# Kernel tuning notes

Hardware: AMD Instinct MI355X
Metric: run time of the kernel (lower is better)

Reference implementation:

```python
import jax, jax.numpy as jnp
import numpy as np

T = 0.2


def _cdist(a, b):
    # Euclidean cdist with zero-safe sqrt (grad 0 at coincident points, like torch)
    d2 = (a * a).sum(-1)[:, None] + (b * b).sum(-1)[None, :] - 2.0 * (a @ b.T)
    d2 = jnp.maximum(d2, 0.0)
    safe = jnp.where(d2 > 0, d2, 1.0)
    return jnp.where(d2 > 0, jnp.sqrt(safe), 0.0)


def _generator(eps, W_in, b_in, W_blk, b_blk, W_out, b_out):
    x = eps @ W_in.T + b_in
    for i in range(W_blk.shape[0]):  # 4 residual MLP blocks
        x = x + jax.nn.relu(x @ W_blk[i].T + b_blk[i])
    return x @ W_out.T + b_out


def setup_inputs() -> dict:
    N, D, H = 4096, 128, 512
    key = jax.random.key(0)
    ks = jax.random.split(key, 16)

    def lin(kw, kb, fan_in, shape_w, shape_b):
        bound = 1.0 / np.sqrt(fan_in)
        W = jax.random.uniform(kw, shape_w, jnp.float32, -bound, bound)
        b = jax.random.uniform(kb, shape_b, jnp.float32, -bound, bound)
        return W, b

    W_in, b_in = lin(ks[0], ks[1], D, (H, D), (H,))
    W_blk, b_blk = lin(ks[2], ks[3], H, (4, H, H), (4, H))
    W_out, b_out = lin(ks[4], ks[5], H, (D, H), (D,))
    y_pos = jax.random.normal(ks[6], (N, D), jnp.float32)
    eps = jax.random.normal(ks[7], (N, D), jnp.float32)
    return {"y_pos": y_pos, "eps": eps, "W_in": W_in, "b_in": b_in,
            "W_blk": W_blk, "b_blk": b_blk, "W_out": W_out, "b_out": b_out}


def reference(y_pos, eps, W_in, b_in, W_blk, b_blk, W_out, b_out):
    x = _generator(eps, W_in, b_in, W_blk, b_blk, W_out, b_out)  # [N, D]
    N = y_pos.shape[0]
    dist_pos = _cdist(x, y_pos)                                   # [N, N]
    dist_neg = _cdist(x, x) + jnp.eye(x.shape[0], dtype=x.dtype) * 1e6
    A = jnp.concatenate([-dist_pos / T, -dist_neg / T], axis=-1)  # [N, 2N]
    A_row = jax.nn.softmax(A, axis=-1)
    A_col = jax.nn.softmax(A, axis=-2)
    A_soft = jnp.sqrt(A_row * A_col)
    A_pos = A_soft[:, :N]
    A_neg = A_soft[:, N:]
    s_pos = A_pos.sum(axis=1, keepdims=True)
    s_neg = A_neg.sum(axis=1, keepdims=True)
    Wpos = A_pos * s_neg
    # torch in-place: Wpos *= s_neg mutates A_pos BEFORE A_pos.sum is taken,
    # so Wneg = A_neg * (A_pos * s_neg).sum(1) = A_neg * s_pos * s_neg
    Wneg = A_neg * (s_pos * s_neg)
    V = Wpos @ y_pos - Wneg @ x                                   # drifting field
    target = jax.lax.stop_gradient(x + V)
    return jnp.mean((x - target) ** 2)
```

## Files before the change

### kernel.cpp

```cpp
#include <hip/hip_runtime.h>
#include <math.h>

#define N 4096
#define D 128
#define H 512
#define KSPLIT 4
#define SC_LOG2 7.2134752044f

typedef short bf16x8 __attribute__((ext_vector_type(8)));
typedef float f32x4 __attribute__((ext_vector_type(4)));
typedef unsigned short u16x8 __attribute__((ext_vector_type(8)));
typedef unsigned short u16;
typedef _Float16 f16;
typedef _Float16 f16x4 __attribute__((ext_vector_type(4)));

#define MFMA(a, b, c) __builtin_amdgcn_mfma_f32_16x16x32_bf16((a), (b), (c), 0, 0, 0)

__device__ __forceinline__ float fexp2(float x)
{
#if __has_builtin(__builtin_amdgcn_exp2f)
    return __builtin_amdgcn_exp2f(x);
#else
    return exp2f(x);
#endif
}

__device__ __forceinline__ float fsqrt(float x)
{
#if __has_builtin(__builtin_amdgcn_sqrtf)
    return __builtin_amdgcn_sqrtf(x);
#else
    return sqrtf(x);
#endif
}

__device__ __forceinline__ float bf2f(u16 h)
{
    return __uint_as_float(((unsigned)h) << 16);
}

__device__ __forceinline__ u16 rtn_bf16(float v)
{
    unsigned u = __float_as_uint(v);
    return (u16)((u + 0x7FFFu + ((u >> 16) & 1u)) >> 16);
}

__device__ __forceinline__ void split1(float v, u16& h, u16& l)
{
    u16 hh = rtn_bf16(v);
    float r = v - bf2f(hh);
    h = hh;
    l = rtn_bf16(r);
}

__device__ __forceinline__ void split1_trunc(float v, u16& h, u16& l)
{
    unsigned bv = __float_as_uint(v);
    unsigned hb = bv & 0xFFFF0000u;
    float r = v - __uint_as_float(hb);
    h = (u16)(hb >> 16);
    l = (u16)(__float_as_uint(r) >> 16);
}

template <int CTRL>
__device__ __forceinline__ float dppf(float x)
{
    int r = __builtin_amdgcn_update_dpp(0, __float_as_int(x), CTRL, 0xF, 0xF, true);
    return __int_as_float(r);
}

struct SplitDesc { const float* src; u16* h; int n; int ks; int os; };
struct SplitArgs { SplitDesc d[4]; };

__global__ __launch_bounds__(256) void split_multi(SplitArgs args)
{
    SplitDesc de = args.d[blockIdx.y];
    int idx = (blockIdx.x * 256 + threadIdx.x) * 4;
    if (idx >= de.n) return;
    float4 v = *(const float4*)(de.src + idx);
    ushort4 hv;
    hv.x = rtn_bf16(v.x); hv.y = rtn_bf16(v.y);
    hv.z = rtn_bf16(v.z); hv.w = rtn_bf16(v.w);
    if (de.ks < 0) {
        *(ushort4*)(de.h + idx) = hv;
    } else {
        const int ks = de.ks, os = de.os;
        const int lsz = 1 << (ks + os);
        const int layer = idx >> (ks + os);
        const int fl = idx & (lsz - 1);
        const int col = fl >> ks;
        const int k = fl & ((1 << ks) - 1);
        const int kt = k >> 5, quad = (k >> 3) & 3, j = k & 7;
        const int pidx = layer * lsz + (((((kt << 2) + quad) << os) + col) << 3) + j;
        *(ushort4*)(de.h + pidx) = hv;
    }
}

template <int K, bool RR>
__device__ __forceinline__ void gen_layer(
    u16 (&XhS)[16][520], u16 (&XlS)[16][520],
    const u16* __restrict__ Wp, const float* __restrict__ bias,
    int w, int quad, int l16)
{
    const int nb = w * 32;
    constexpr int NT = K >> 5;
    f32x4 acc[2] = {};
    float bl2[2];
    bl2[0] = bias[nb + l16];
    bl2[1] = bias[nb + 16 + l16];
    const u16* wb = Wp + (size_t)quad * 4096 + (size_t)nb * 8 + (size_t)l16 * 8;
    #pragma unroll
    for (int kc = 0; kc < NT / 2; ++kc) {
        const int kta = 2 * kc, ktb = 2 * kc + 1;
        bf16x8 b0[2], b1[2];
        b0[0] = *(const bf16x8*)(wb + kta * 16384);
        b0[1] = *(const bf16x8*)(wb + kta * 16384 + 128);
        b1[0] = *(const bf16x8*)(wb + ktb * 16384);
        b1[1] = *(const bf16x8*)(wb + ktb * 16384 + 128);
        bf16x8 a0h = *(const bf16x8*)&XhS[l16][kta * 32 + quad * 8];
        bf16x8 a0l = *(const bf16x8*)&XlS[l16][kta * 32 + quad * 8];
        bf16x8 a1h = *(const bf16x8*)&XhS[l16][ktb * 32 + quad * 8];
        bf16x8 a1l = *(const bf16x8*)&XlS[l16][ktb * 32 + quad * 8];
        acc[0] = MFMA(a0h, b0[0], acc[0]);
        acc[0] = MFMA(a0l, b0[0], acc[0]);
        acc[1] = MFMA(a0h, b0[1], acc[1]);
        acc[1] = MFMA(a0l, b0[1], acc[1]);
        acc[0] = MFMA(a1h, b1[0], acc[0]);
        acc[0] = MFMA(a1l, b1[0], acc[0]);
        acc[1] = MFMA(a1h, b1[1], acc[1]);
        acc[1] = MFMA(a1l, b1[1], acc[1]);
    }
    __syncthreads();
    #pragma unroll
    for (int ni = 0; ni < 2; ++ni) {
        const int col = nb + ni * 16 + l16;
        #pragma unroll
        for (int r = 0; r < 4; ++r) {
            const int row = quad * 4 + r;
            float v = acc[ni][r] + bl2[ni];
            if (RR) {
                float prev = bf2f(XhS[row][col]) + bf2f(XlS[row][col]);
                v = prev + fmaxf(v, 0.0f);
            }
            u16 hh, ll;
            split1_trunc(v, hh, ll);
            XhS[row][col] = hh;
            XlS[row][col] = ll;
        }
    }
    __syncthreads();
}

__global__ __launch_bounds__(1024) void gen_fused(
    const float* __restrict__ eps,
    const u16* __restrict__ Win, const u16* __restrict__ Wblk,
    const u16* __restrict__ Wout,
    const float* __restrict__ b_in, const float* __restrict__ b_blk,
    const float* __restrict__ b_out,
    float* __restrict__ xo, u16* __restrict__ xh)
{
    __shared__ u16 XhS[16][520], XlS[16][520];
    const int t = threadIdx.x;
    const int w = t >> 6, lane = t & 63;
    const int quad = lane >> 4, l16 = lane & 15;
    const int bm = blockIdx.x * 16;

    {
        int idx = t * 2;
        int row = idx >> 7, col = idx & 127;
        float2 v = *(const float2*)(eps + (size_t)(bm + row) * D + col);
        ushort2 hv, lv;
        split1(v.x, hv.x, lv.x); split1(v.y, hv.y, lv.y);
        *(ushort2*)&XhS[row][col] = hv;
        *(ushort2*)&XlS[row][col] = lv;
    }
    __syncthreads();

    gen_layer<D, false>(XhS, XlS, Win, b_in, w, quad, l16);
    #pragma unroll 1
    for (int i = 0; i < 4; ++i)
        gen_layer<H, true>(XhS, XlS, Wblk + (size_t)i * H * H, b_blk + i * H,
                           w, quad, l16);

    if (w < 8) {
        const int n0 = w * 16;
        constexpr int NT = H >> 5;
        f32x4 acc5 = {};
        const float bl = b_out[n0 + l16];
        const u16* wb = Wout + (size_t)quad * 1024 + (size_t)n0 * 8
                             + (size_t)l16 * 8;
        #pragma unroll
        for (int kc = 0; kc < NT / 2; ++kc) {
            const int kta = 2 * kc, ktb = 2 * kc + 1;
            bf16x8 b0 = *(const bf16x8*)(wb + kta * 4096);
            bf16x8 b1 = *(const bf16x8*)(wb + ktb * 4096);
            bf16x8 a0h = *(const bf16x8*)&XhS[l16][kta * 32 + quad * 8];
            bf16x8 a0l = *(const bf16x8*)&XlS[l16][kta * 32 + quad * 8];
            bf16x8 a1h = *(const bf16x8*)&XhS[l16][ktb * 32 + quad * 8];
            bf16x8 a1l = *(const bf16x8*)&XlS[l16][ktb * 32 + quad * 8];
            acc5 = MFMA(a0h, b0, acc5);
            acc5 = MFMA(a0l, b0, acc5);
            acc5 = MFMA(a1h, b1, acc5);
            acc5 = MFMA(a1l, b1, acc5);
        }
        const int col = n0 + l16;
        #pragma unroll
        for (int r = 0; r < 4; ++r) {
            const int gm = bm + quad * 4 + r;
            float v = acc5[r] + bl;
            xo[(size_t)gm * D + col] = v;
            xh[(size_t)gm * D + col] = rtn_bf16(v);
        }
    }
}

__global__ __launch_bounds__(256) void rownorm(
    const float* __restrict__ X, const float* __restrict__ Y,
    float* __restrict__ nx, float* __restrict__ ny)
{
    const float* src = blockIdx.y ? Y : X;
    float* dst = blockIdx.y ? ny : nx;
    const int t = threadIdx.x;
    const int row = blockIdx.x * 64 + (t >> 2);
    const int q = t & 3;
    const float* rp = src + (size_t)row * D + q * 32;
    float s = 0.f;
    #pragma unroll
    for (int i = 0; i < 8; ++i) {
        float4 v = *(const float4*)(rp + i * 4);
        s += v.x * v.x + v.y * v.y + v.z * v.z + v.w * v.w;
    }
    s += __shfl_xor(s, 1);
    s += __shfl_xor(s, 2);
    if (q == 0) dst[row] = s;
}

__global__ __launch_bounds__(256) void transpose_rtn(
    const float* __restrict__ X, const float* __restrict__ Y,
    u16* __restrict__ Xth, u16* __restrict__ Yth)
{
    const float* src = blockIdx.z ? Y : X;
    u16* th = blockIdx.z ? Yth : Xth;
    __shared__ float tile[32][33];
    const int t = threadIdx.x;
    const int r0 = blockIdx.x * 32, c0 = blockIdx.y * 32;
    {
        int rit = t >> 3, coff = (t & 7) * 4;
        float4 v = *(const float4*)(src + (size_t)(r0 + rit) * D + c0 + coff);
        tile[rit][coff + 0] = v.x; tile[rit][coff + 1] = v.y;
        tile[rit][coff + 2] = v.z; tile[rit][coff + 3] = v.w;
    }
    __syncthreads();
    {
        int cit = t >> 3, roff = (t & 7) * 4;
        ushort4 hv;
        hv.x = rtn_bf16(tile[roff + 0][cit]);
        hv.y = rtn_bf16(tile[roff + 1][cit]);
        hv.z = rtn_bf16(tile[roff + 2][cit]);
        hv.w = rtn_bf16(tile[roff + 3][cit]);
        *(ushort4*)(th + (size_t)(c0 + cit) * N + r0 + roff) = hv;
    }
}

__global__ __launch_bounds__(256) void dist_fused(
    const u16* __restrict__ Xh, const u16* __restrict__ Yh,
    const float* __restrict__ nx, const float* __restrict__ ny,
    f16* __restrict__ Apos, f16* __restrict__ Aneg,
    float* __restrict__ prm_p, float* __restrict__ prs_p,
    float* __restrict__ pcm_p, float* __restrict__ pcs_p,
    float* __restrict__ prm_n, float* __restrict__ prs_n)
{
    const int mat = blockIdx.z;
    const u16* Bhp = mat ? Xh : Yh;
    const float* nb = mat ? nx : ny;
    f16* Out = mat ? Aneg : Apos;
    float* prm = mat ? prm_n : prm_p;
    float* prs = mat ? prs_n : prs_p;

    __shared__ u16 XhS[128][40], YhS[128][40];
    const int t = threadIdx.x;
    const int w = t >> 6, lane = t & 63;
    const int quad = lane >> 4, l16 = lane & 15;
    const int bm = blockIdx.y * 128, bn = blockIdx.x * 128;
    f32x4 acc[2][8] = {};

    for (int k0 = 0; k0 < D; k0 += 32) {
        __syncthreads();
        #pragma unroll
        for (int p = 0; p < 2; ++p) {
            int slot = t + p * 256;
            int row = slot >> 2, koff = (slot & 3) << 3;
            *(u16x8*)&XhS[row][koff] =
                *(const u16x8*)(Xh + (size_t)(bm + row) * D + k0 + koff);
        }
        #pragma unroll
        for (int p = 0; p < 2; ++p) {
            int slot = t + p * 256;
            int row = slot >> 2, koff = (slot & 3) << 3;
            int pr = ((row & 3) << 4) | ((row & 63) >> 2) | (row & 64);
            int kf = koff ^ (((pr >> 4) & 3) << 3);
            *(u16x8*)&YhS[pr][kf] =
                *(const u16x8*)(Bhp + (size_t)(bn + row) * D + k0 + koff);
        }
        __syncthreads();
        bf16x8 af[2], bhf[8];
        #pragma unroll
        for (int mi = 0; mi < 2; ++mi)
            af[mi] = *(const bf16x8*)&XhS[w * 32 + mi * 16 + l16][quad * 8];
        #pragma unroll
        for (int ni = 0; ni < 8; ++ni) {
            int nn = ni & 3, hf = ni >> 2;
            bhf[ni] = *(const bf16x8*)
                &YhS[hf * 64 + nn * 16 + l16][(quad * 8) ^ (nn << 3)];
        }
        #pragma unroll
        for (int mi = 0; mi < 2; ++mi)
            #pragma unroll
            for (int ni = 0; ni < 8; ++ni)
                acc[mi][ni] = MFMA(af[mi], bhf[ni], acc[mi][ni]);
    }
    const int jb = bn + (l16 << 2);
    const float SC2 = SC_LOG2 * SC_LOG2;
    const float c2 = -2.0f * SC2;
    const float4 n0v = *(const float4*)(nb + jb);
    const float4 n1v = *(const float4*)(nb + jb + 64);
    const float nl[8] = {n0v.x * SC2, n0v.y * SC2, n0v.z * SC2, n0v.w * SC2,
                         n1v.x * SC2, n1v.y * SC2, n1v.z * SC2, n1v.w * SC2};
    #pragma unroll
    for (int mi = 0; mi < 2; ++mi)
        #pragma unroll
        for (int r = 0; r < 4; ++r) {
            const int gm = bm + w * 32 + mi * 16 + quad * 4 + r;
            const float nxm = nx[gm] * SC2;
            f16x4 ov0, ov1;
            #pragma unroll
            for (int nn = 0; nn < 4; ++nn) {
                float s0 = fsqrt(fmaxf(
                    fmaf(acc[mi][nn][r], c2, nxm + nl[nn]), 0.f));
                float s1 = fsqrt(fmaxf(
                    fmaf(acc[mi][4 + nn][r], c2, nxm + nl[4 + nn]), 0.f));
                if (mat) {
                    if (gm == jb + nn) s0 = 5.0e6f;
                    if (gm == jb + 64 + nn) s1 = 5.0e6f;
                }
                acc[mi][nn][r] = s0;
                acc[mi][4 + nn][r] = s1;
                ov0[nn] = (f16)(-s0);
                ov1[nn] = (f16)(-s1);
            }
            *(f16x4*)(Out + (size_t)gm * N + jb) = ov0;
            *(f16x4*)(Out + (size_t)gm * N + jb + 64) = ov1;
        }
    float m[2][4];
    #pragma unroll
    for (int mi = 0; mi < 2; ++mi)
        #pragma unroll
        for (int r = 0; r < 4; ++r) {
            float v = fminf(fminf(fminf(acc[mi][0][r], acc[mi][1][r]),
                                  fminf(acc[mi][2][r], acc[mi][3][r])),
                            fminf(fminf(acc[mi][4][r], acc[mi][5][r]),
                                  fminf(acc[mi][6][r], acc[mi][7][r])));
            v = fminf(v, dppf<0xB1>(v));
            v = fminf(v, dppf<0x4E>(v));
            v = fminf(v, dppf<0x141>(v));
            v = fminf(v, dppf<0x140>(v));
            m[mi][r] = v;
        }
    float mn = fminf(fminf(fminf(m[0][0], m[0][1]), fminf(m[0][2], m[0][3])),
                     fminf(fminf(m[1][0], m[1][1]), fminf(m[1][2], m[1][3])));
    mn = fminf(mn, __shfl_xor(mn, 16));
    mn = fminf(mn, __shfl_xor(mn, 32));
    float sig[2][4] = {};
    float cs[8] = {};
    #pragma unroll
    for (int mi = 0; mi < 2; ++mi)
        #pragma unroll
        for (int ni = 0; ni < 8; ++ni) {
            float e0 = fexp2(mn - acc[mi][ni][0]);
            float e1 = fexp2(mn - acc[mi][ni][1]);
            float e2 = fexp2(mn - acc[mi][ni][2]);
            float e3 = fexp2(mn - acc[mi][ni][3]);
            sig[mi][0] += e0; sig[mi][1] += e1;
            sig[mi][2] += e2; sig[mi][3] += e3;
            cs[ni] += (e0 + e1) + (e2 + e3);
        }
    const int ct = blockIdx.x;
    #pragma unroll
    for (int mi = 0; mi < 2; ++mi)
        #pragma unroll
        for (int r = 0; r < 4; ++r) {
            float s = sig[mi][r];
            s += dppf<0xB1>(s);
            s += dppf<0x4E>(s);
            s += dppf<0x141>(s);
            s += dppf<0x140>(s);
            s *= fexp2(m[mi][r] - mn);
            if (l16 == 0) {
                int grow = bm + w * 32 + mi * 16 + quad * 4 + r;
                prm[(size_t)ct * N + grow] = -m[mi][r];
                prs[(size_t)ct * N + grow] = s;
            }
        }
    if (mat == 0) {
        const int rt = blockIdx.y * 4 + w;
        #pragma unroll
        for (int ni = 0; ni < 8; ++ni) {
            cs[ni] += __shfl_xor(cs[ni], 16);
            cs[ni] += __shfl_xor(cs[ni], 32);
        }
        if (quad == 0) {
            float4 c0 = {cs[0], cs[1], cs[2], cs[3]};
            float4 c1 = {cs[4], cs[5], cs[6], cs[7]};
            float4 m4 = {-mn, -mn, -mn, -mn};
            *(float4*)(pcs_p + (size_t)rt * N + jb) = c0;
            *(float4*)(pcs_p + (size_t)rt * N + jb + 64) = c1;
            *(float4*)(pcm_p + (size_t)rt * N + jb) = m4;
            *(float4*)(pcm_p + (size_t)rt * N + jb + 64) = m4;
        }
    }
}

__global__ __launch_bounds__(256) void stats_combine(
    const float* __restrict__ prm_p, const float* __restrict__ prs_p,
    const float* __restrict__ prm_n, const float* __restrict__ prs_n,
    const float* __restrict__ pcm_p, const float* __restrict__ pcs_p,
    float* __restrict__ m_row, float* __restrict__ isr,
    float* __restrict__ m_col, float* __restrict__ isc)
{
    __shared__ float Ms[4][64], Ss[4][64];
    const int t = threadIdx.x;
    const int g = t >> 6, l = t & 63;
    const int idx = blockIdx.x * 64 + l;

    float m = -3.0e38f, s = 0.f;
    if (idx < N) {
        const int i = idx;
        const int c0 = g * 8;
        #pragma unroll 4
        for (int c = c0; c < c0 + 8; ++c) {
            m = fmaxf(m, prm_p[(size_t)c * N + i]);
            m = fmaxf(m, prm_n[(size_t)c * N + i]);
        }
        #pragma unroll 4
        for (int c = c0; c < c0 + 8; ++c) {
            s += prs_p[(size_t)c * N + i] * fexp2(prm_p[(size_t)c * N + i] - m);
            s += prs_n[(size_t)c * N + i] * fexp2(prm_n[(size_t)c * N + i] - m);
        }
    } else {
        const int mat = (idx - N) >> 12;
        const int j = idx & (N - 1);
        const float* pm = mat ? prm_n : pcm_p;
        const float* ps = mat ? prs_n : pcs_p;
        const int cnt = mat ? 8 : 32;
        const int cb = g * cnt;
        #pragma unroll 4
        for (int c = cb; c < cb + cnt; ++c)
            m = fmaxf(m, pm[(size_t)c * N + j]);
        #pragma unroll 4
        for (int c = cb; c < cb + cnt; ++c)
            s += ps[(size_t)c * N + j] * fexp2(pm[(size_t)c * N + j] - m);
    }
    Ms[g][l] = m; Ss[g][l] = s;
    __syncthreads();
    if (g == 0) {
        float m0 = Ms[0][l], m1 = Ms[1][l], m2 = Ms[2][l], m3 = Ms[3][l];
        float mm = fmaxf(fmaxf(m0, m1), fmaxf(m2, m3));
        float ss = Ss[0][l] * fexp2(m0 - mm) + Ss[1][l] * fexp2(m1 - mm)
                 + Ss[2][l] * fexp2(m2 - mm) + Ss[3][l] * fexp2(m3 - mm);
        if (idx < N) {
            m_row[idx] = mm;
            isr[idx] = 1.0f / sqrtf(ss);
        } else {
            const int mat = (idx - N) >> 12;
            const int j = idx & (N - 1);
            m_col[mat * N + j] = mm;
            isc[mat * N + j] = 1.0f / sqrtf(ss);
        }
    }
}

__global__ __launch_bounds__(256) void pv_mfma(
    const f16* __restrict__ Apos, const f16* __restrict__ Aneg,
    const u16* __restrict__ Yth, const u16* __restrict__ Xth,
    const float* __restrict__ m_row, const float* __restrict__ isr,
    const float* __restrict__ m_col, const float* __restrict__ isc,
    float* __restrict__ u_part, float* __restrict__ w_part,
    float* __restrict__ sp_part, float* __restrict__ sn_part)
{
    const int mat = blockIdx.z;
    const f16* Am = mat ? Aneg : Apos;
    const u16* Bh = mat ? Xth : Yth;
    const float* mc = m_col + mat * N;
    const float* ic = isc + mat * N;
    float* Cp = (mat ? w_part : u_part) + (size_t)blockIdx.y * (N * D);
    float* spn = (mat ? sn_part : sp_part) + (size_t)blockIdx.y * N;

    __shared__ u16 BhS[128][72];
    __shared__ u16 PhS[64][72], PlS[64][72];
    __shared__ float mrS[64], isrS[64];

    const int t = threadIdx.x;
    const int w = t >> 6, lane = t & 63;
    const int quad = lane >> 4, l16 = lane & 15;
    const int bm = blockIdx.x * 64;
    const int jbase = blockIdx.y * (N / KSPLIT);
    const int arow = t >> 4;
    const int aj = (t & 15) << 2;

    if (t < 64) { mrS[t] = m_row[bm + t]; isrS[t] = isr[bm + t]; }

    f32x4 acc[8] = {};
    float rs[4] = {0.f, 0.f, 0.f, 0.f};

    for (int jt = 0; jt < (N / KSPLIT) / 64; ++jt) {
        const int j0 = jbase + jt * 64;
        __syncthreads();
        #pragma unroll
        for (int p = 0; p < 4; ++p) {
            int slot = t + p * 256;
            int d = slot >> 3, joff = (slot & 7) << 3;
            *(u16x8*)&BhS[d][joff] = *(const u16x8*)(Bh + (size_t)d * N + j0 + joff);
        }
        float4 mcv = *(const float4*)(mc + j0 + aj);
        float4 icv = *(const float4*)(ic + j0 + aj);
        #pragma unroll
        for (int s = 0; s < 4; ++s) {
            int row = arow + s * 16;
            f16x4 av = *(const f16x4*)(Am + (size_t)(bm + row) * N + j0 + aj);
            float mr = mrS[row], sr = isrS[row];
            float p0 = fexp2((float)av.x - 0.5f * (mr + mcv.x)) * (sr * icv.x);
            float p1 = fexp2((float)av.y - 0.5f * (mr + mcv.y)) * (sr * icv.y);
            float p2 = fexp2((float)av.z - 0.5f * (mr + mcv.z)) * (sr * icv.z);
            float p3 = fexp2((float)av.w - 0.5f * (mr + mcv.w)) * (sr * icv.w);
            rs[s] += p0 + p1 + p2 + p3;
            ushort4 hv, lv;
            split1_trunc(p0, hv.x, lv.x); split1_trunc(p1, hv.y, lv.y);
            split1_trunc(p2, hv.z, lv.z); split1_trunc(p3, hv.w, lv.w);
            *(ushort4*)&PhS[row][aj] = hv;
            *(ushort4*)&PlS[row][aj] = lv;
        }
        __syncthreads();
        #pragma unroll
        for (int ks = 0; ks < 2; ++ks) {
            const int kk = ks * 32 + quad * 8;
            bf16x8 ph = *(const bf16x8*)&PhS[w * 16 + l16][kk];
            bf16x8 pl = *(const bf16x8*)&PlS[w * 16 + l16][kk];
            #pragma unroll
            for (int ni = 0; ni < 8; ++ni) {
                bf16x8 bh = *(const bf16x8*)&BhS[ni * 16 + l16][kk];
                acc[ni] = MFMA(ph, bh, acc[ni]);
                acc[ni] = MFMA(pl, bh, acc[ni]);
            }
        }
    }
    #pragma unroll
    for (int ni = 0; ni < 8; ++ni)
        #pragma unroll
        for (int r = 0; r < 4; ++r) {
            int row = w * 16 + quad * 4 + r;
            int col = ni * 16 + l16;
            Cp[(size_t)(bm + row) * D + col] = acc[ni][r];
        }
    #pragma unroll
    for (int s = 0; s < 4; ++s) {
        float v = rs[s];
        v += __shfl_xor(v, 1); v += __shfl_xor(v, 2);
        v += __shfl_xor(v, 4); v += __shfl_xor(v, 8);
        if (l16 == 0) spn[bm + arow + s * 16] = v;
    }
}

__global__ __launch_bounds__(256) void final_reduce(const float* __restrict__ u_part,
    const float* __restrict__ w_part, const float* __restrict__ sp_part,
    const float* __restrict__ sn_part, double* __restrict__ acc_part)
{
    __shared__ float red[256];
    const int t = threadIdx.x;
    const int idx = blockIdx.x * 256 + t;
    float u = 0.f, w = 0.f;
    #pragma unroll
    for (int c = 0; c < KSPLIT; ++c) {
        u += u_part[(size_t)c * (N * D) + idx];
        w += w_part[(size_t)c * (N * D) + idx];
    }
    const int i = idx >> 7;
    float sp = 0.f, sn = 0.f;
    #pragma unroll
    for (int c = 0; c < KSPLIT; ++c) {
        sp += sp_part[(size_t)c * N + i];
        sn += sn_part[(size_t)c * N + i];
    }
    const float v = sn * u - sp * sn * w;
    red[t] = v * v; __syncthreads();
    for (int s = 128; s > 0; s >>= 1) { if (t < s) red[t] += red[t + s]; __syncthreads(); }
    if (!t) acc_part[blockIdx.x] = (double)red[0];
}

__global__ __launch_bounds__(256) void finalize(const double* __restrict__ acc_part,
                                                float* __restrict__ out)
{
    __shared__ double red[256];
    const int t = threadIdx.x;
    double s = 0.0;
    #pragma unroll
    for (int i = 0; i < 8; ++i) s += acc_part[t + i * 256];
    red[t] = s; __syncthreads();
    for (int st = 128; st > 0; st >>= 1) {
        if (t < st) red[t] += red[t + st];
        __syncthreads();
    }
    if (!t) out[0] = (float)(red[0] * (1.0 / ((double)N * (double)D)));
}

extern "C" void kernel_launch(void* const* d_in, const int* in_sizes, int n_in,
                              void* d_out, int out_size, void* d_ws, size_t ws_size,
                              hipStream_t stream)
{
    const float* y_pos = (const float*)d_in[0];
    const float* eps   = (const float*)d_in[1];
    const float* W_in  = (const float*)d_in[2];
    const float* b_in  = (const float*)d_in[3];
    const float* W_blk = (const float*)d_in[4];
    const float* b_blk = (const float*)d_in[5];
    const float* W_out = (const float*)d_in[6];
    const float* b_out = (const float*)d_in[7];
    float* out = (float*)d_out;
    (void)in_sizes; (void)n_in; (void)out_size; (void)ws_size;

    char* p = (char*)d_ws;
    auto alloc = [&](size_t bytes) {
        char* r = p;
        p += (bytes + 255) & ~(size_t)255;
        return r;
    };
    double* acc_part = (double*)alloc(2048 * 8);
    float* sp_part = (float*)alloc((size_t)KSPLIT * N * 4);
    float* sn_part = (float*)alloc((size_t)KSPLIT * N * 4);
    float* m_row  = (float*)alloc(N * 4);
    float* isr    = (float*)alloc(N * 4);
    float* m_col  = (float*)alloc(2 * N * 4);
    float* isc    = (float*)alloc(2 * N * 4);
    float* nx     = (float*)alloc(N * 4);
    float* ny     = (float*)alloc(N * 4);
    float* xo  = (float*)alloc((size_t)N * D * 4);
    u16* xh    = (u16*)alloc((size_t)N * D * 2);
    u16* xth   = (u16*)alloc((size_t)N * D * 2);
    u16* yh    = (u16*)alloc((size_t)N * D * 2);
    u16* yth   = (u16*)alloc((size_t)N * D * 2);
    char* genreg = alloc((size_t)KSPLIT * N * D * 4 * 2);
    u16* wih = (u16*)genreg;
    u16* wbh = wih + (size_t)H * D;
    u16* woh = wbh + (size_t)4 * H * H;
    float* prm_p = (float*)genreg;
    float* prs_p = prm_p + 32 * N;
    float* prm_n = prs_p + 32 * N;
    float* prs_n = prm_n + 32 * N;
    float* pcm_p = prs_n + 32 * N;
    float* pcs_p = pcm_p + 128 * N;
    float* u_part = (float*)genreg;
    float* w_part = u_part + (size_t)KSPLIT * N * D;
    f16* Apos = (f16*)alloc((size_t)N * N * 2);
    f16* Aneg = (f16*)alloc((size_t)N * N * 2);

    SplitArgs sa;
    sa.d[0] = { y_pos, yh,  N * D,     -1, 0 };
    sa.d[1] = { W_in,  wih, H * D,      7, 9 };
    sa.d[2] = { W_blk, wbh, 4 * H * H,  9, 9 };
    sa.d[3] = { W_out, woh, D * H,      9, 7 };
    split_multi<<<dim3(1024, 4), 256, 0, stream>>>(sa);

    gen_fused<<<N / 16, 1024, 0, stream>>>(eps, wih, wbh, woh,
                                           b_in, b_blk, b_out, xo, xh);

    rownorm<<<dim3(N / 64, 2), 256, 0, stream>>>(xo, y_pos, nx, ny);

    transpose_rtn<<<dim3(N / 32, D / 32, 2), 256, 0, stream>>>(
        xo, y_pos, xth, yth);

    dist_fused<<<dim3(N / 128, N / 128, 2), 256, 0, stream>>>(
        xh, yh, nx, ny, Apos, Aneg,
        prm_p, prs_p, pcm_p, pcs_p, prm_n, prs_n);

    stats_combine<<<192, 256, 0, stream>>>(prm_p, prs_p, prm_n, prs_n,
                                           pcm_p, pcs_p,
                                           m_row, isr, m_col, isc);

    pv_mfma<<<dim3(N / 64, KSPLIT, 2), 256, 0, stream>>>(Apos, Aneg,
        yth, xth, m_row, isr, m_col, isc, u_part, w_part, sp_part, sn_part);

    final_reduce<<<(N * D) / 256, 256, 0, stream>>>(u_part, w_part,
                                                    sp_part, sn_part, acc_part);
    finalize<<<1, 256, 0, stream>>>(acc_part, out);
}
```

Baseline: 191.4 us.

## Recompute distance tiles in pv_mfma instead of storing fp16 A matrices

Removes the two N×N fp16 distance matrices written by dist_fused and read back by pv_mfma. pv_mfma now recomputes each 64x64 distance tile with bf16 MFMAs from the X/Y rows and norms before the softmax-weighted PV product. This trades about 64MB of HBM write/read traffic for a second distance GEMM, with B-operand fragments loaded directly from global memory without LDS staging. The distance is no longer rounded to fp16 before the exponential, which slightly changes numerics.

```diff
diff --git a/kernel.cpp b/kernel.cpp
--- a/kernel.cpp
+++ b/kernel.cpp
@@ -11,8 +11,6 @@
 typedef float f32x4 __attribute__((ext_vector_type(4)));
 typedef unsigned short u16x8 __attribute__((ext_vector_type(8)));
 typedef unsigned short u16;
-typedef _Float16 f16;
-typedef _Float16 f16x4 __attribute__((ext_vector_type(4)));
 
 #define MFMA(a, b, c) __builtin_amdgcn_mfma_f32_16x16x32_bf16((a), (b), (c), 0, 0, 0)
 
@@ -265,7 +263,6 @@
 __global__ __launch_bounds__(256) void dist_fused(
     const u16* __restrict__ Xh, const u16* __restrict__ Yh,
     const float* __restrict__ nx, const float* __restrict__ ny,
-    f16* __restrict__ Apos, f16* __restrict__ Aneg,
     float* __restrict__ prm_p, float* __restrict__ prs_p,
     float* __restrict__ pcm_p, float* __restrict__ pcs_p,
     float* __restrict__ prm_n, float* __restrict__ prs_n)
@@ -273,7 +270,6 @@
     const int mat = blockIdx.z;
     const u16* Bhp = mat ? Xh : Yh;
     const float* nb = mat ? nx : ny;
-    f16* Out = mat ? Aneg : Apos;
     float* prm = mat ? prm_n : prm_p;
     float* prs = mat ? prs_n : prs_p;
 
@@ -332,7 +328,6 @@
         for (int r = 0; r < 4; ++r) {
             const int gm = bm + w * 32 + mi * 16 + quad * 4 + r;
             const float nxm = nx[gm] * SC2;
-            f16x4 ov0, ov1;
             #pragma unroll
             for (int nn = 0; nn < 4; ++nn) {
                 float s0 = fsqrt(fmaxf(
@@ -345,11 +340,7 @@
                 }
                 acc[mi][nn][r] = s0;
                 acc[mi][4 + nn][r] = s1;
-                ov0[nn] = (f16)(-s0);
-                ov1[nn] = (f16)(-s1);
             }
-            *(f16x4*)(Out + (size_t)gm * N + jb) = ov0;
-            *(f16x4*)(Out + (size_t)gm * N + jb + 64) = ov1;
         }
     float m[2][4];
     #pragma unroll
@@ -480,16 +471,18 @@
 }
 
 __global__ __launch_bounds__(256) void pv_mfma(
-    const f16* __restrict__ Apos, const f16* __restrict__ Aneg,
+    const u16* __restrict__ Xh, const u16* __restrict__ Yh,
     const u16* __restrict__ Yth, const u16* __restrict__ Xth,
+    const float* __restrict__ nx, const float* __restrict__ ny,
     const float* __restrict__ m_row, const float* __restrict__ isr,
     const float* __restrict__ m_col, const float* __restrict__ isc,
     float* __restrict__ u_part, float* __restrict__ w_part,
     float* __restrict__ sp_part, float* __restrict__ sn_part)
 {
     const int mat = blockIdx.z;
-    const f16* Am = mat ? Aneg : Apos;
+    const u16* Zh = mat ? Xh : Yh;
     const u16* Bh = mat ? Xth : Yth;
+    const float* nb = mat ? nx : ny;
     const float* mc = m_col + mat * N;
     const float* ic = isc + mat * N;
     float* Cp = (mat ? w_part : u_part) + (size_t)blockIdx.y * (N * D);
@@ -497,17 +490,29 @@
 
     __shared__ u16 BhS[128][72];
     __shared__ u16 PhS[64][72], PlS[64][72];
-    __shared__ float mrS[64], isrS[64];
 
     const int t = threadIdx.x;
     const int w = t >> 6, lane = t & 63;
     const int quad = lane >> 4, l16 = lane & 15;
     const int bm = blockIdx.x * 64;
     const int jbase = blockIdx.y * (N / KSPLIT);
-    const int arow = t >> 4;
-    const int aj = (t & 15) << 2;
-
-    if (t < 64) { mrS[t] = m_row[bm + t]; isrS[t] = isr[bm + t]; }
+    const float SC2 = SC_LOG2 * SC_LOG2;
+    const float c2 = -2.0f * SC2;
+
+    bf16x8 axf[4];
+    #pragma unroll
+    for (int kt = 0; kt < 4; ++kt)
+        axf[kt] = *(const bf16x8*)
+            (Xh + (size_t)(bm + w * 16 + l16) * D + kt * 32 + quad * 8);
+
+    const int rbase = bm + w * 16 + quad * 4;
+    float nxr[4], mr4[4], sr4[4];
+    #pragma unroll
+    for (int r = 0; r < 4; ++r) {
+        nxr[r] = nx[rbase + r] * SC2;
+        mr4[r] = m_row[rbase + r];
+        sr4[r] = isr[rbase + r];
+    }
 
     f32x4 acc[8] = {};
     float rs[4] = {0.f, 0.f, 0.f, 0.f};
@@ -521,24 +526,38 @@
             int d = slot >> 3, joff = (slot & 7) << 3;
             *(u16x8*)&BhS[d][joff] = *(const u16x8*)(Bh + (size_t)d * N + j0 + joff);
         }
-        float4 mcv = *(const float4*)(mc + j0 + aj);
-        float4 icv = *(const float4*)(ic + j0 + aj);
-        #pragma unroll
-        for (int s = 0; s < 4; ++s) {
-            int row = arow + s * 16;
-            f16x4 av = *(const f16x4*)(Am + (size_t)(bm + row) * N + j0 + aj);
-            float mr = mrS[row], sr = isrS[row];
-            float p0 = fexp2((float)av.x - 0.5f * (mr + mcv.x)) * (sr * icv.x);
-            float p1 = fexp2((float)av.y - 0.5f * (mr + mcv.y)) * (sr * icv.y);
-            float p2 = fexp2((float)av.z - 0.5f * (mr + mcv.z)) * (sr * icv.z);
-            float p3 = fexp2((float)av.w - 0.5f * (mr + mcv.w)) * (sr * icv.w);
-            rs[s] += p0 + p1 + p2 + p3;
-            ushort4 hv, lv;
-            split1_trunc(p0, hv.x, lv.x); split1_trunc(p1, hv.y, lv.y);
-            split1_trunc(p2, hv.z, lv.z); split1_trunc(p3, hv.w, lv.w);
-            *(ushort4*)&PhS[row][aj] = hv;
-            *(ushort4*)&PlS[row][aj] = lv;
-        }
+        f32x4 sacc[4] = {};
+        #pragma unroll
+        for (int kt = 0; kt < 4; ++kt)
+            #pragma unroll
+            for (int ni = 0; ni < 4; ++ni) {
+                bf16x8 bz = *(const bf16x8*)
+                    (Zh + (size_t)(j0 + ni * 16 + l16) * D + kt * 32 + quad * 8);
+                sacc[ni] = MFMA(axf[kt], bz, sacc[ni]);
+            }
+        float nlj[4], mcj[4], icj[4];
+        #pragma unroll
+        for (int ni = 0; ni < 4; ++ni) {
+            const int j = j0 + ni * 16 + l16;
+            nlj[ni] = nb[j] * SC2;
+            mcj[ni] = mc[j];
+            icj[ni] = ic[j];
+        }
+        #pragma unroll
+        for (int ni = 0; ni < 4; ++ni)
+            #pragma unroll
+            for (int r = 0; r < 4; ++r) {
+                float s = fsqrt(fmaxf(
+                    fmaf(sacc[ni][r], c2, nxr[r] + nlj[ni]), 0.f));
+                if (mat && (rbase + r == j0 + ni * 16 + l16)) s = 5.0e6f;
+                float pv = fexp2(-s - 0.5f * (mr4[r] + mcj[ni]))
+                         * (sr4[r] * icj[ni]);
+                rs[r] += pv;
+                u16 hh, ll;
+                split1_trunc(pv, hh, ll);
+                PhS[w * 16 + quad * 4 + r][ni * 16 + l16] = hh;
+                PlS[w * 16 + quad * 4 + r][ni * 16 + l16] = ll;
+            }
         __syncthreads();
         #pragma unroll
         for (int ks = 0; ks < 2; ++ks) {
@@ -562,11 +581,11 @@
             Cp[(size_t)(bm + row) * D + col] = acc[ni][r];
         }
     #pragma unroll
-    for (int s = 0; s < 4; ++s) {
-        float v = rs[s];
+    for (int r = 0; r < 4; ++r) {
+        float v = rs[r];
         v += __shfl_xor(v, 1); v += __shfl_xor(v, 2);
         v += __shfl_xor(v, 4); v += __shfl_xor(v, 8);
-        if (l16 == 0) spn[bm + arow + s * 16] = v;
+        if (l16 == 0) spn[rbase + r] = v;
     }
 }
 
@@ -659,8 +678,6 @@
     float* pcs_p = pcm_p + 128 * N;
     float* u_part = (float*)genreg;
     float* w_part = u_part + (size_t)KSPLIT * N * D;
-    f16* Apos = (f16*)alloc((size_t)N * N * 2);
-    f16* Aneg = (f16*)alloc((size_t)N * N * 2);
 
     SplitArgs sa;
     sa.d[0] = { y_pos, yh,  N * D,     -1, 0 };
@@ -678,15 +695,16 @@
         xo, y_pos, xth, yth);
 
     dist_fused<<<dim3(N / 128, N / 128, 2), 256, 0, stream>>>(
-        xh, yh, nx, ny, Apos, Aneg,
+        xh, yh, nx, ny,
         prm_p, prs_p, pcm_p, pcs_p, prm_n, prs_n);
 
     stats_combine<<<192, 256, 0, stream>>>(prm_p, prs_p, prm_n, prs_n,
                                            pcm_p, pcs_p,
                                            m_row, isr, m_col, isc);
 
-    pv_mfma<<<dim3(N / 64, KSPLIT, 2), 256, 0, stream>>>(Apos, Aneg,
-        yth, xth, m_row, isr, m_col, isc, u_part, w_part, sp_part, sn_part);
+    pv_mfma<<<dim3(N / 64, KSPLIT, 2), 256, 0, stream>>>(
+        xh, yh, yth, xth, nx, ny,
+        m_row, isr, m_col, isc, u_part, w_part, sp_part, sn_part);
 
     final_reduce<<<(N * D) / 256, 256, 0, stream>>>(u_part, w_part,
                                                     sp_part, sn_part, acc_part);
```

Result: slower. 271.0 us (+41.6%).
